# Kernel optimization log

Hardware: AMD Instinct MI355X
Metric: run time of the kernel (lower is better)

## Reference

```python
import jax, jax.numpy as jnp
import numpy as np

N_NODES = 100000
N_EDGES = 1600000
IN_F = 128
OUT_F = 64
ORDER = 3


def setup_inputs() -> dict:
    key = jax.random.key(0)
    k1, k2, k3, k4, k5 = jax.random.split(key, 5)
    x = jax.random.normal(k1, (N_NODES, IN_F), dtype=jnp.float32)
    edge_index = jax.random.randint(k2, (2, N_EDGES), 0, N_NODES, dtype=jnp.int64)
    edge_weight = jax.random.uniform(k3, (N_EDGES,), dtype=jnp.float32)
    # nn.Linear default init scale ~ 1/sqrt(in_features)
    W_weight = jax.random.normal(k4, (OUT_F, IN_F), dtype=jnp.float32) / np.sqrt(IN_F)
    W_bias = jax.random.normal(k5, (OUT_F,), dtype=jnp.float32) / np.sqrt(IN_F)
    return {"x": x, "edge_index": edge_index, "edge_weight": edge_weight,
            "W_weight": W_weight, "W_bias": W_bias}


def _spmm(edge_index, edge_weight, h):
    # out[dst] = sum_e edge_weight[e] * h[src[e]]
    src, dst = edge_index[0], edge_index[1]
    msg = edge_weight[:, None] * h[src]          # [E, OUT_F] gathered messages
    return jax.ops.segment_sum(msg, dst, num_segments=N_NODES)


def reference(x, edge_index, edge_weight, W_weight, W_bias):
    # Linear projection: [N, IN_F] -> [N, OUT_F]
    h = x @ W_weight.T + W_bias
    # `order` hops of sparse propagation
    for _ in range(ORDER):
        h = _spmm(edge_index, edge_weight, h)
    return h
```

## Files before the change

### kernel.cpp

```cpp
#include <hip/hip_runtime.h>
#include <hip/hip_fp16.h>

#define N_NODES_C 100000
#define N_EDGES_C 1600000
#define IN_F 128
#define OUT_F 64

#define BIN_SHIFT 9
#define BIN_SZ    512
#define NBIN      ((N_NODES_C + BIN_SZ - 1) / BIN_SZ)
#define NCHUNK    256
#define CH        (N_EDGES_C / NCHUNK)

#define GEMM_BLOCKS ((N_NODES_C + 1023) / 1024)
#define SROW 72

typedef __attribute__((ext_vector_type(8))) _Float16 half8;
typedef __attribute__((ext_vector_type(4))) float    f32x4;

__global__ __launch_bounds__(1024) void fused_gemm_hist_kernel(
    const float* __restrict__ x, const float* __restrict__ W,
    const float* __restrict__ bias, _Float16* __restrict__ h, int n,
    const int* __restrict__ dst, int* __restrict__ hist) {
  __shared__ __align__(16) _Float16 sout[16 * 16 * SROW];
  __shared__ int hh[NBIN];
  const int t = threadIdx.x;

  if (blockIdx.x >= GEMM_BLOCKS) {
    const int c = blockIdx.x - GEMM_BLOCKS;
    for (int i = t; i < NBIN; i += 1024) hh[i] = 0;
    __syncthreads();
    const int e0 = c * CH;
    for (int i = t; i < CH; i += 1024)
      atomicAdd(&hh[dst[e0 + i] >> BIN_SHIFT], 1);
    __syncthreads();
    for (int i = t; i < NBIN; i += 1024)
      hist[i * NCHUNK + c] = hh[i];
    return;
  }

  const int wid  = t >> 6;
  const int lane = t & 63;
  const int lr   = lane & 15;
  const int lg   = lane >> 4;
  const int wbase = (blockIdx.x * 16 + wid) * 64;
  if (wbase >= n) return;

  half8 bfrag[4][4];
#pragma unroll
  for (int nc = 0; nc < 4; ++nc) {
    const float* wrow = W + (size_t)(nc * 16 + lr) * IN_F + lg * 8;
#pragma unroll
    for (int kc = 0; kc < 4; ++kc) {
      float4 a = ((const float4*)(wrow + kc * 32))[0];
      float4 b = ((const float4*)(wrow + kc * 32))[1];
      half8 f;
      f[0] = (_Float16)a.x; f[1] = (_Float16)a.y;
      f[2] = (_Float16)a.z; f[3] = (_Float16)a.w;
      f[4] = (_Float16)b.x; f[5] = (_Float16)b.y;
      f[6] = (_Float16)b.z; f[7] = (_Float16)b.w;
      bfrag[nc][kc] = f;
    }
  }

  float bv[4];
#pragma unroll
  for (int nc = 0; nc < 4; ++nc) bv[nc] = bias[nc * 16 + lr];

  _Float16* sw = sout + wid * 16 * SROW;

#pragma unroll
  for (int ti = 0; ti < 4; ++ti) {
    const int node0 = wbase + ti * 16;
    if (node0 >= n) break;

    int ra = node0 + lr;
    if (ra >= n) ra = n - 1;
    const float* xp = x + (size_t)ra * IN_F + lg * 8;

    f32x4 acc[4] = {{0.f, 0.f, 0.f, 0.f}, {0.f, 0.f, 0.f, 0.f},
                    {0.f, 0.f, 0.f, 0.f}, {0.f, 0.f, 0.f, 0.f}};
#pragma unroll
    for (int kc = 0; kc < 4; ++kc) {
      float4 a = ((const float4*)(xp + kc * 32))[0];
      float4 b = ((const float4*)(xp + kc * 32))[1];
      half8 af;
      af[0] = (_Float16)a.x; af[1] = (_Float16)a.y;
      af[2] = (_Float16)a.z; af[3] = (_Float16)a.w;
      af[4] = (_Float16)b.x; af[5] = (_Float16)b.y;
      af[6] = (_Float16)b.z; af[7] = (_Float16)b.w;
#pragma unroll
      for (int nc = 0; nc < 4; ++nc)
        acc[nc] = __builtin_amdgcn_mfma_f32_16x16x32_f16(af, bfrag[nc][kc], acc[nc], 0, 0, 0);
    }

#pragma unroll
    for (int nc = 0; nc < 4; ++nc)
#pragma unroll
      for (int r = 0; r < 4; ++r)
        sw[(lg * 4 + r) * SROW + nc * 16 + lr] = (_Float16)(acc[nc][r] + bv[nc]);
#pragma unroll
    for (int it = 0; it < 2; ++it) {
      int rl = (lane >> 3) + it * 8;
      int node = node0 + rl;
      if (node < n)
        ((uint4*)(h + (size_t)node * OUT_F))[lane & 7] =
            ((const uint4*)(sw + rl * SROW))[lane & 7];
    }
  }
}

__global__ __launch_bounds__(1024) void scan_all_kernel(
    const int* __restrict__ hist, int* __restrict__ soff,
    int* __restrict__ binStart) {
  __shared__ int s[256];
  const int t = threadIdx.x;
  int total = 0;
  if (t < NBIN) {
    const int* row = hist + (size_t)t * NCHUNK;
    for (int c = 0; c < NCHUNK; ++c) total += row[c];
  }
  if (t < 256) s[t] = (t < NBIN) ? total : 0;
  __syncthreads();
  for (int off = 1; off < 256; off <<= 1) {
    int u = 0;
    if (t < 256 && t >= off) u = s[t - off];
    __syncthreads();
    if (t < 256) s[t] += u;
    __syncthreads();
  }
  if (t < NBIN) {
    int base = s[t] - total;
    binStart[t] = base;
    const int* row = hist + (size_t)t * NCHUNK;
    int* so = soff + (size_t)t * NCHUNK;
    int run = base;
    for (int c = 0; c < NCHUNK; ++c) { so[c] = run; run += row[c]; }
  }
}

__global__ __launch_bounds__(1024) void binscatter_kernel(
    const int* __restrict__ src, const int* __restrict__ dst,
    const float* __restrict__ w, const int* __restrict__ soff,
    int* __restrict__ stage_d, int2* __restrict__ stage_sw) {
  __shared__ int lcur[NBIN];
  const int t = threadIdx.x;
  const int c = blockIdx.x;
  for (int i = t; i < NBIN; i += 1024) lcur[i] = soff[i * NCHUNK + c];
  __syncthreads();
  const int e0 = c * CH;
  for (int i = t; i < CH; i += 1024) {
    int e = e0 + i;
    int d = dst[e];
    int p = atomicAdd(&lcur[d >> BIN_SHIFT], 1);
    stage_d[p]  = d;
    stage_sw[p] = make_int2(src[e] * OUT_F, __float_as_int(w[e]));
  }
}

__global__ __launch_bounds__(1024) void place_kernel(
    const int* __restrict__ binStart, const int* __restrict__ stage_d,
    const int2* __restrict__ stage_sw, int* __restrict__ row_ptr,
    int2* __restrict__ edges, int n) {
  __shared__ int lcount[BIN_SZ];
  __shared__ int s[BIN_SZ];
  __shared__ int lcur[BIN_SZ];
  const int t = threadIdx.x;
  const int b = blockIdx.x;
  const int base = binStart[b];
  const int end  = (b == NBIN - 1) ? N_EDGES_C : binStart[b + 1];
  const int node0 = b << BIN_SHIFT;

  if (t < BIN_SZ) lcount[t] = 0;
  __syncthreads();
  for (int i = base + t; i < end; i += 1024)
    atomicAdd(&lcount[stage_d[i] - node0], 1);
  __syncthreads();

  int v = 0;
  if (t < BIN_SZ) { v = lcount[t]; s[t] = v; }
  __syncthreads();
  for (int off = 1; off < BIN_SZ; off <<= 1) {
    int u = (t < BIN_SZ && t >= off) ? s[t - off] : 0;
    __syncthreads();
    if (t < BIN_SZ) s[t] += u;
    __syncthreads();
  }
  if (t < BIN_SZ) {
    int ex = base + s[t] - v;
    int node = node0 + t;
    if (node < n) row_ptr[node] = ex;
    lcur[t] = ex;
  }
  __syncthreads();

  for (int i = base + t; i < end; i += 1024) {
    int d = stage_d[i];
    int p = atomicAdd(&lcur[d - node0], 1);
    edges[p] = stage_sw[i];
  }
  if (b == NBIN - 1 && t == 0) row_ptr[n] = N_EDGES_C;
}

__device__ inline void fma8_h(float* acc, uint4 r, float w) {
  unsigned u[4] = {r.x, r.y, r.z, r.w};
#pragma unroll
  for (int q = 0; q < 4; ++q) {
    __half2 h2 = *reinterpret_cast<__half2*>(&u[q]);
    float2 f = __half22float2(h2);
    acc[2 * q + 0] += w * f.x;
    acc[2 * q + 1] += w * f.y;
  }
}

template <int OUT32>
__global__ __launch_bounds__(256) void spmm16_kernel(
    const int* __restrict__ row_ptr, const int2* __restrict__ edges,
    const __half* __restrict__ hin, void* __restrict__ hout, int n) {
  const int node = blockIdx.x * 32 + (threadIdx.x >> 3);
  const int fl   = threadIdx.x & 7;
  if (node >= n) return;
  const int beg = row_ptr[node];
  const int end = row_ptr[node + 1];

  float acc[8] = {0.f, 0.f, 0.f, 0.f, 0.f, 0.f, 0.f, 0.f};
  int j = beg;
  for (; j + 3 < end; j += 4) {
    int2 e0 = edges[j + 0];
    int2 e1 = edges[j + 1];
    int2 e2 = edges[j + 2];
    int2 e3 = edges[j + 3];
    uint4 r0 = ((const uint4*)(hin + e0.x))[fl];
    uint4 r1 = ((const uint4*)(hin + e1.x))[fl];
    uint4 r2 = ((const uint4*)(hin + e2.x))[fl];
    uint4 r3 = ((const uint4*)(hin + e3.x))[fl];
    fma8_h(acc, r0, __int_as_float(e0.y));
    fma8_h(acc, r1, __int_as_float(e1.y));
    fma8_h(acc, r2, __int_as_float(e2.y));
    fma8_h(acc, r3, __int_as_float(e3.y));
  }
  for (; j < end; ++j) {
    int2 e = edges[j];
    uint4 r = ((const uint4*)(hin + e.x))[fl];
    fma8_h(acc, r, __int_as_float(e.y));
  }

  if (OUT32) {
    float* op = (float*)hout + (size_t)node * OUT_F + 8 * fl;
    ((float4*)op)[0] = make_float4(acc[0], acc[1], acc[2], acc[3]);
    ((float4*)op)[1] = make_float4(acc[4], acc[5], acc[6], acc[7]);
  } else {
    union { __half2 h2[4]; uint4 u; } pk;
#pragma unroll
    for (int q = 0; q < 4; ++q)
      pk.h2[q] = __floats2half2_rn(acc[2 * q], acc[2 * q + 1]);
    ((uint4*)((char*)hout + (size_t)node * 128))[fl] = pk.u;
  }
}

extern "C" void kernel_launch(void* const* d_in, const int* in_sizes, int n_in,
                              void* d_out, int out_size, void* d_ws, size_t ws_size,
                              hipStream_t stream) {
  const float* x    = (const float*)d_in[0];
  const int*   ei   = (const int*)d_in[1];
  const float* ew   = (const float*)d_in[2];
  const float* W    = (const float*)d_in[3];
  const float* bias = (const float*)d_in[4];
  float* out = (float*)d_out;

  const int N = N_NODES_C;
  const int E = N_EDGES_C;
  const int* src = ei;
  const int* dst = ei + E;
  const int NH = NBIN * NCHUNK;

  char* p = (char*)d_ws;
  auto carve = [&](size_t bytes) {
    void* r = (void*)p;
    p += (bytes + 255) & ~(size_t)255;
    return r;
  };
  __half* h16A     = (__half*)carve((size_t)N * OUT_F * 2);
  __half* h16B     = (__half*)carve((size_t)N * OUT_F * 2);
  int*   row_ptr   = (int*)  carve((size_t)(N + 1) * 4);
  int2*  edges     = (int2*) carve((size_t)E * 8);
  int*   hist      = (int*)  carve((size_t)NH * 4);
  int*   soff      = (int*)  carve((size_t)NH * 4);
  int*   binStart  = (int*)  carve((size_t)(NBIN + 1) * 4);

  int2* stage_sw = (int2*)d_out;
  int*  stage_d  = (int*)((char*)d_out + (size_t)E * 8);

  fused_gemm_hist_kernel<<<GEMM_BLOCKS + NCHUNK, 1024, 0, stream>>>(
      x, W, bias, (_Float16*)h16A, N, dst, hist);
  scan_all_kernel<<<1, 1024, 0, stream>>>(hist, soff, binStart);
  binscatter_kernel<<<NCHUNK, 1024, 0, stream>>>(src, dst, ew, soff, stage_d, stage_sw);
  place_kernel<<<NBIN, 1024, 0, stream>>>(binStart, stage_d, stage_sw,
                                          row_ptr, edges, N);
  spmm16_kernel<0><<<(N + 31) / 32, 256, 0, stream>>>(row_ptr, edges, h16A, h16B, N);
  spmm16_kernel<0><<<(N + 31) / 32, 256, 0, stream>>>(row_ptr, edges, h16B, h16A, N);
  spmm16_kernel<1><<<(N + 31) / 32, 256, 0, stream>>>(row_ptr, edges, h16A, out, N);
}
```

Before: 301.7 us.

## Split fused GEMM/histogram kernel and parallelize bin scan with wave shuffles

Un-fuses the projection GEMM from the destination histogram: the GEMM now runs as its own kernel with 256-thread blocks (4 waves) and the histogram as a separate launch. The single-block scan now uses one wavefront per bin with int4 loads and shuffle reductions and scans, instead of one serial thread looping over 256 chunks per bin. The serial per-bin loops were the main latency in the scan kernel. The cost is one extra kernel launch and the loss of overlap between GEMM and histogram work.

```diff
diff --git a/kernel.cpp b/kernel.cpp
--- a/kernel.cpp
+++ b/kernel.cpp
@@ -12,38 +12,21 @@
 #define NCHUNK    256
 #define CH        (N_EDGES_C / NCHUNK)
 
-#define GEMM_BLOCKS ((N_NODES_C + 1023) / 1024)
 #define SROW 72
 
 typedef __attribute__((ext_vector_type(8))) _Float16 half8;
 typedef __attribute__((ext_vector_type(4))) float    f32x4;
 
-__global__ __launch_bounds__(1024) void fused_gemm_hist_kernel(
+__global__ __launch_bounds__(256) void gemm_mfma_kernel(
     const float* __restrict__ x, const float* __restrict__ W,
-    const float* __restrict__ bias, _Float16* __restrict__ h, int n,
-    const int* __restrict__ dst, int* __restrict__ hist) {
-  __shared__ __align__(16) _Float16 sout[16 * 16 * SROW];
-  __shared__ int hh[NBIN];
-  const int t = threadIdx.x;
-
-  if (blockIdx.x >= GEMM_BLOCKS) {
-    const int c = blockIdx.x - GEMM_BLOCKS;
-    for (int i = t; i < NBIN; i += 1024) hh[i] = 0;
-    __syncthreads();
-    const int e0 = c * CH;
-    for (int i = t; i < CH; i += 1024)
-      atomicAdd(&hh[dst[e0 + i] >> BIN_SHIFT], 1);
-    __syncthreads();
-    for (int i = t; i < NBIN; i += 1024)
-      hist[i * NCHUNK + c] = hh[i];
-    return;
-  }
-
+    const float* __restrict__ bias, _Float16* __restrict__ h, int n) {
+  __shared__ __align__(16) _Float16 sout[4 * 16 * SROW];
+  const int t    = threadIdx.x;
   const int wid  = t >> 6;
   const int lane = t & 63;
   const int lr   = lane & 15;
   const int lg   = lane >> 4;
-  const int wbase = (blockIdx.x * 16 + wid) * 64;
+  const int wbase = (blockIdx.x * 4 + wid) * 64;
   if (wbase >= n) return;
 
   half8 bfrag[4][4];
@@ -110,32 +93,70 @@
   }
 }
 
+__global__ __launch_bounds__(1024) void hist_kernel(
+    const int* __restrict__ dst, int* __restrict__ hist) {
+  __shared__ int h[NBIN];
+  const int t = threadIdx.x;
+  for (int i = t; i < NBIN; i += 1024) h[i] = 0;
+  __syncthreads();
+  const int e0 = blockIdx.x * CH;
+  for (int i = t; i < CH; i += 1024)
+    atomicAdd(&h[dst[e0 + i] >> BIN_SHIFT], 1);
+  __syncthreads();
+  for (int i = t; i < NBIN; i += 1024)
+    hist[i * NCHUNK + blockIdx.x] = h[i];
+}
+
 __global__ __launch_bounds__(1024) void scan_all_kernel(
     const int* __restrict__ hist, int* __restrict__ soff,
     int* __restrict__ binStart) {
-  __shared__ int s[256];
+  __shared__ __align__(16) int binTot[256];
+  __shared__ __align__(16) int binBase[256];
   const int t = threadIdx.x;
-  int total = 0;
-  if (t < NBIN) {
-    const int* row = hist + (size_t)t * NCHUNK;
-    for (int c = 0; c < NCHUNK; ++c) total += row[c];
-  }
-  if (t < 256) s[t] = (t < NBIN) ? total : 0;
-  __syncthreads();
-  for (int off = 1; off < 256; off <<= 1) {
-    int u = 0;
-    if (t < 256 && t >= off) u = s[t - off];
-    __syncthreads();
-    if (t < 256) s[t] += u;
-    __syncthreads();
-  }
-  if (t < NBIN) {
-    int base = s[t] - total;
-    binStart[t] = base;
-    const int* row = hist + (size_t)t * NCHUNK;
-    int* so = soff + (size_t)t * NCHUNK;
-    int run = base;
-    for (int c = 0; c < NCHUNK; ++c) { so[c] = run; run += row[c]; }
+  const int w = t >> 6, lane = t & 63;
+
+  for (int b = w; b < NBIN; b += 16) {
+    int4 v = ((const int4*)(hist + (size_t)b * NCHUNK))[lane];
+    int s = v.x + v.y + v.z + v.w;
+#pragma unroll
+    for (int off = 1; off < 64; off <<= 1) s += __shfl_xor(s, off);
+    if (lane == 0) binTot[b] = s;
+  }
+  if (t >= NBIN && t < 256) binTot[t] = 0;
+  __syncthreads();
+
+  if (w == 0) {
+    int4 v = ((const int4*)binTot)[lane];
+    int s0 = v.x, s1 = s0 + v.y, s2 = s1 + v.z, s3 = s2 + v.w;
+    int ls = s3;
+#pragma unroll
+    for (int off = 1; off < 64; off <<= 1) {
+      int u = __shfl_up(ls, off);
+      if (lane >= off) ls += u;
+    }
+    int ex = ls - s3;
+    int4 o;
+    o.x = ex; o.y = ex + s0; o.z = ex + s1; o.w = ex + s2;
+    ((int4*)binBase)[lane] = o;
+  }
+  __syncthreads();
+
+  if (t < NBIN) binStart[t] = binBase[t];
+
+  for (int b = w; b < NBIN; b += 16) {
+    int base = binBase[b];
+    int4 v = ((const int4*)(hist + (size_t)b * NCHUNK))[lane];
+    int s0 = v.x, s1 = s0 + v.y, s2 = s1 + v.z, s3 = s2 + v.w;
+    int ls = s3;
+#pragma unroll
+    for (int off = 1; off < 64; off <<= 1) {
+      int u = __shfl_up(ls, off);
+      if (lane >= off) ls += u;
+    }
+    int ex = base + ls - s3;
+    int4 o;
+    o.x = ex; o.y = ex + s0; o.z = ex + s1; o.w = ex + s2;
+    ((int4*)(soff + (size_t)b * NCHUNK))[lane] = o;
   }
 }
 
@@ -291,12 +312,12 @@
   int2* stage_sw = (int2*)d_out;
   int*  stage_d  = (int*)((char*)d_out + (size_t)E * 8);
 
-  fused_gemm_hist_kernel<<<GEMM_BLOCKS + NCHUNK, 1024, 0, stream>>>(
-      x, W, bias, (_Float16*)h16A, N, dst, hist);
-  scan_all_kernel<<<1, 1024, 0, stream>>>(hist, soff, binStart);
+  gemm_mfma_kernel<<<(N + 255) / 256, 256, 0, stream>>>(x, W, bias, (_Float16*)h16A, N);
+  hist_kernel      <<<NCHUNK, 1024, 0, stream>>>(dst, hist);
+  scan_all_kernel  <<<1, 1024, 0, stream>>>(hist, soff, binStart);
   binscatter_kernel<<<NCHUNK, 1024, 0, stream>>>(src, dst, ew, soff, stage_d, stage_sw);
-  place_kernel<<<NBIN, 1024, 0, stream>>>(binStart, stage_d, stage_sw,
-                                          row_ptr, edges, N);
+  place_kernel     <<<NBIN, 1024, 0, stream>>>(binStart, stage_d, stage_sw,
+                                               row_ptr, edges, N);
   spmm16_kernel<0><<<(N + 31) / 32, 256, 0, stream>>>(row_ptr, edges, h16A, h16B, N);
   spmm16_kernel<0><<<(N + 31) / 32, 256, 0, stream>>>(row_ptr, edges, h16B, h16A, N);
   spmm16_kernel<1><<<(N + 31) / 32, 256, 0, stream>>>(row_ptr, edges, h16A, out, N);
```

After: 278.7 us. 1.08x faster.
